# Kernel optimization log

Measured on AMD Instinct MI355X. Metric: run time of the kernel, lower is better.

The kernel has to match this reference:

```python
import jax, jax.numpy as jnp
import numpy as np

N_NODES = 100000


def _gcn_propagate(x, src, dst, n):
    """Symmetric-normalized propagation with self-loops (PyG gcn_norm, K=1).

    out[dst] += deg^-1/2[src] * deg^-1/2[dst] * x[src], including self-loops.
    """
    loop = jnp.arange(n, dtype=src.dtype)
    s = jnp.concatenate([src, loop])
    d = jnp.concatenate([dst, loop])
    deg = jax.ops.segment_sum(jnp.ones_like(d, dtype=x.dtype), d, num_segments=n)
    dinv = jnp.where(deg > 0, jax.lax.rsqrt(deg), jnp.zeros_like(deg))
    norm = dinv[s] * dinv[d]            # [E+N]
    msg = x[s] * norm[:, None]          # [E+N, F] gathered messages
    return jax.ops.segment_sum(msg, d, num_segments=n)


def setup_inputs() -> dict:
    key = jax.random.key(0)
    ks = jax.random.split(key, 6)
    n, e, f, h, c = N_NODES, 1600000, 64, 64, 16
    x = jax.random.normal(ks[0], (n, f), dtype=jnp.float32)
    edge_index = jax.random.randint(ks[1], (2, e), 0, n, dtype=jnp.int64)
    W1 = jax.random.normal(ks[2], (h, f), dtype=jnp.float32) * 0.1
    b1 = jnp.zeros((h,), dtype=jnp.float32)
    W2 = jax.random.normal(ks[3], (h, h), dtype=jnp.float32) * 0.1
    b2 = jnp.zeros((h,), dtype=jnp.float32)
    W3 = jax.random.normal(ks[4], (c, h), dtype=jnp.float32) * 0.1
    b3 = jnp.zeros((c,), dtype=jnp.float32)
    return {"x": x, "edge_index": edge_index, "W1": W1, "b1": b1,
            "W2": W2, "b2": b2, "W3": W3, "b3": b3}


def reference(x, edge_index, W1, b1, W2, b2, W3, b3):
    n = x.shape[0]
    src, dst = edge_index[0], edge_index[1]
    # SGConv 1 (K=1): propagate then linear; dropout is identity in eval mode
    h = _gcn_propagate(x, src, dst, n) @ W1.T + b1
    h = jax.nn.relu(h)
    # SGConv 2
    h = _gcn_propagate(h, src, dst, n) @ W2.T + b2
    h = jax.nn.relu(h)
    # final linear
    return h @ W3.T + b3
```

## Files before the change

### kernel.cpp

```cpp
#include <hip/hip_runtime.h>
#include <hip/hip_fp16.h>


#define F 64
#define C 16
#define SCAN_B 1024

__device__ __forceinline__ float rl(float v, int l) {
    return __uint_as_float(__builtin_amdgcn_readlane(__float_as_uint(v), l));
}

__device__ __forceinline__ float4 unpack_h4(unsigned long long raw) {
    __half2 lo = __builtin_bit_cast(__half2, (unsigned int)(raw & 0xffffffffull));
    __half2 hi = __builtin_bit_cast(__half2, (unsigned int)(raw >> 32));
    float2 f0 = __half22float2(lo);
    float2 f1 = __half22float2(hi);
    return make_float4(f0.x, f0.y, f1.x, f1.y);
}

__global__ void degrank_kernel(const int* __restrict__ dst, int* __restrict__ deg,
                               int* __restrict__ rank, int E) {
    int i = (blockIdx.x * blockDim.x + threadIdx.x) * 4;
    if (i + 4 <= E) {
        int4 d = *(const int4*)(dst + i);
        int4 r;
        r.x = atomicAdd(&deg[d.x], 1);
        r.y = atomicAdd(&deg[d.y], 1);
        r.z = atomicAdd(&deg[d.z], 1);
        r.w = atomicAdd(&deg[d.w], 1);
        *(int4*)(rank + i) = r;
    } else {
        for (int k = i; k < E; ++k) rank[k] = atomicAdd(&deg[dst[k]], 1);
    }
}

__global__ __launch_bounds__(256) void scan1_kernel(const int* __restrict__ deg,
                                                    int* __restrict__ part,
                                                    int* __restrict__ bsum, int n) {
    __shared__ int ts[256];
    int b = blockIdx.x, t = threadIdx.x;
    int base = b * SCAN_B + t * 4;
    int v[4], sum = 0;
#pragma unroll
    for (int k = 0; k < 4; ++k) { int i = base + k; v[k] = (i < n) ? deg[i] : 0; sum += v[k]; }
    ts[t] = sum;
    __syncthreads();
    for (int off = 1; off < 256; off <<= 1) {
        int add = (t >= off) ? ts[t - off] : 0;
        __syncthreads();
        ts[t] += add;
        __syncthreads();
    }
    int run = ts[t] - sum;
#pragma unroll
    for (int k = 0; k < 4; ++k) { int i = base + k; if (i < n) part[i] = run; run += v[k]; }
    if (t == 255) bsum[b] = ts[255];
}

__global__ __launch_bounds__(256) void scan2_kernel(int* __restrict__ bsum, int nb) {
    __shared__ int ts[256];
    int t = threadIdx.x;
    int v = (t < nb) ? bsum[t] : 0;
    ts[t] = v;
    __syncthreads();
    for (int off = 1; off < 256; off <<= 1) {
        int add = (t >= off) ? ts[t - off] : 0;
        __syncthreads();
        ts[t] += add;
        __syncthreads();
    }
    if (t < nb) bsum[t] = ts[t] - v;
}

__global__ void scan3_kernel(const int* __restrict__ part, const int* __restrict__ bsum,
                             const int* __restrict__ deg, int* __restrict__ rowptr,
                             float* __restrict__ dinv, int n, int E) {
    int i = blockIdx.x * blockDim.x + threadIdx.x;
    if (i < n) {
        rowptr[i] = part[i] + bsum[i / SCAN_B];
        dinv[i] = rsqrtf((float)deg[i] + 1.0f);
    }
    if (i == 0) rowptr[n] = E;
}

__global__ void fill_kernel(const int* __restrict__ src, const int* __restrict__ dst,
                            const int* __restrict__ rank, const int* __restrict__ rowptr,
                            int* __restrict__ csr_src, int E) {
    int i = (blockIdx.x * blockDim.x + threadIdx.x) * 4;
    if (i + 4 <= E) {
        int4 s = *(const int4*)(src + i);
        int4 d = *(const int4*)(dst + i);
        int4 r = *(const int4*)(rank + i);
        csr_src[rowptr[d.x] + r.x] = s.x;
        csr_src[rowptr[d.y] + r.y] = s.y;
        csr_src[rowptr[d.z] + r.z] = s.z;
        csr_src[rowptr[d.w] + r.w] = s.w;
    } else {
        for (int k = i; k < E; ++k) csr_src[rowptr[dst[k]] + rank[k]] = src[k];
    }
}

__global__ __launch_bounds__(256) void gemm1_kernel(
    const float4* __restrict__ in4, const float* __restrict__ W,
    const float* __restrict__ scale, __half* __restrict__ yout, int n) {
    int tid = threadIdx.x;
    int lane = tid & 63;
    int m = lane & 15;
    float4 w[16];
#pragma unroll
    for (int t = 0; t < 16; ++t) w[t] = *(const float4*)(W + (size_t)lane * F + 4 * t);
    int gw = blockIdx.x * 4 + (tid >> 6);
    int nw = gridDim.x * 4;
    int node = gw;
    if (node >= n) return;
    float4 v = in4[(size_t)node * 16 + m];
    while (true) {
        int nxt = node + nw;
        float4 vn;
        if (nxt < n) vn = in4[(size_t)nxt * 16 + m];
        float acc = 0.0f;
#pragma unroll
        for (int t = 0; t < 16; ++t) {
            acc = fmaf(rl(v.x, t), w[t].x, acc);
            acc = fmaf(rl(v.y, t), w[t].y, acc);
            acc = fmaf(rl(v.z, t), w[t].z, acc);
            acc = fmaf(rl(v.w, t), w[t].w, acc);
        }
        acc *= scale[node];
        yout[(size_t)node * F + lane] = __float2half(acc);
        if (nxt >= n) break;
        v = vn;
        node = nxt;
    }
}

__global__ __launch_bounds__(256) void gemm2_kernel(
    const unsigned long long* __restrict__ in8, const float* __restrict__ W,
    __half* __restrict__ yout, int n) {
    int tid = threadIdx.x;
    int lane = tid & 63;
    int m = lane & 15;
    float4 w[16];
#pragma unroll
    for (int t = 0; t < 16; ++t) w[t] = *(const float4*)(W + (size_t)lane * F + 4 * t);
    int gw = blockIdx.x * 4 + (tid >> 6);
    int nw = gridDim.x * 4;
    int node = gw;
    if (node >= n) return;
    float4 v = unpack_h4(in8[(size_t)node * 16 + m]);
    while (true) {
        int nxt = node + nw;
        float4 vn;
        if (nxt < n) vn = unpack_h4(in8[(size_t)nxt * 16 + m]);
        float acc = 0.0f;
#pragma unroll
        for (int t = 0; t < 16; ++t) {
            acc = fmaf(rl(v.x, t), w[t].x, acc);
            acc = fmaf(rl(v.y, t), w[t].y, acc);
            acc = fmaf(rl(v.z, t), w[t].z, acc);
            acc = fmaf(rl(v.w, t), w[t].w, acc);
        }
        yout[(size_t)node * F + lane] = __float2half(acc);
        if (nxt >= n) break;
        v = vn;
        node = nxt;
    }
}

#define GATHER_CORE(YTAB)                                                     \
    float4 gacc0 = {0,0,0,0}, gacc1 = {0,0,0,0};                              \
    float4 gacc2 = {0,0,0,0}, gacc3 = {0,0,0,0};                              \
    int p = beg;                                                              \
    if (p + 8 <= end) {                                                       \
        int i0 = csr_src[p],     i1 = csr_src[p + 1];                         \
        int i2 = csr_src[p + 2], i3 = csr_src[p + 3];                         \
        int i4 = csr_src[p + 4], i5 = csr_src[p + 5];                         \
        int i6 = csr_src[p + 6], i7 = csr_src[p + 7];                         \
        while (true) {                                                        \
            unsigned long long r0 = YTAB[(size_t)i0 * 16 + m];                \
            unsigned long long r1 = YTAB[(size_t)i1 * 16 + m];                \
            unsigned long long r2 = YTAB[(size_t)i2 * 16 + m];                \
            unsigned long long r3 = YTAB[(size_t)i3 * 16 + m];                \
            unsigned long long r4 = YTAB[(size_t)i4 * 16 + m];                \
            unsigned long long r5 = YTAB[(size_t)i5 * 16 + m];                \
            unsigned long long r6 = YTAB[(size_t)i6 * 16 + m];                \
            unsigned long long r7 = YTAB[(size_t)i7 * 16 + m];                \
            int np = p + 8;                                                   \
            bool more = np + 8 <= end;                                        \
            if (more) {                                                       \
                i0 = csr_src[np];     i1 = csr_src[np + 1];                   \
                i2 = csr_src[np + 2]; i3 = csr_src[np + 3];                   \
                i4 = csr_src[np + 4]; i5 = csr_src[np + 5];                   \
                i6 = csr_src[np + 6]; i7 = csr_src[np + 7];                   \
            }                                                                 \
            float4 v0 = unpack_h4(r0), v1 = unpack_h4(r1);                    \
            float4 v2 = unpack_h4(r2), v3 = unpack_h4(r3);                    \
            float4 v4 = unpack_h4(r4), v5 = unpack_h4(r5);                    \
            float4 v6 = unpack_h4(r6), v7 = unpack_h4(r7);                    \
            gacc0.x += v0.x + v4.x; gacc0.y += v0.y + v4.y;                   \
            gacc0.z += v0.z + v4.z; gacc0.w += v0.w + v4.w;                   \
            gacc1.x += v1.x + v5.x; gacc1.y += v1.y + v5.y;                   \
            gacc1.z += v1.z + v5.z; gacc1.w += v1.w + v5.w;                   \
            gacc2.x += v2.x + v6.x; gacc2.y += v2.y + v6.y;                   \
            gacc2.z += v2.z + v6.z; gacc2.w += v2.w + v6.w;                   \
            gacc3.x += v3.x + v7.x; gacc3.y += v3.y + v7.y;                   \
            gacc3.z += v3.z + v7.z; gacc3.w += v3.w + v7.w;                   \
            p = np;                                                           \
            if (!more) break;                                                 \
        }                                                                     \
    }                                                                         \
    if (p + 4 <= end) {                                                       \
        int i0 = csr_src[p], i1 = csr_src[p + 1];                             \
        int i2 = csr_src[p + 2], i3 = csr_src[p + 3];                         \
        float4 v0 = unpack_h4(YTAB[(size_t)i0 * 16 + m]);                     \
        float4 v1 = unpack_h4(YTAB[(size_t)i1 * 16 + m]);                     \
        float4 v2 = unpack_h4(YTAB[(size_t)i2 * 16 + m]);                     \
        float4 v3 = unpack_h4(YTAB[(size_t)i3 * 16 + m]);                     \
        gacc0.x += v0.x; gacc0.y += v0.y; gacc0.z += v0.z; gacc0.w += v0.w;   \
        gacc1.x += v1.x; gacc1.y += v1.y; gacc1.z += v1.z; gacc1.w += v1.w;   \
        gacc2.x += v2.x; gacc2.y += v2.y; gacc2.z += v2.z; gacc2.w += v2.w;   \
        gacc3.x += v3.x; gacc3.y += v3.y; gacc3.z += v3.z; gacc3.w += v3.w;   \
        p += 4;                                                               \
    }                                                                         \
    for (; p < end; ++p) {                                                    \
        float4 v = unpack_h4(YTAB[(size_t)csr_src[p] * 16 + m]);              \
        gacc0.x += v.x; gacc0.y += v.y; gacc0.z += v.z; gacc0.w += v.w;       \
    }                                                                         \
    float4 a;                                                                 \
    a.x = gacc0.x + gacc1.x + gacc2.x + gacc3.x;                              \
    a.y = gacc0.y + gacc1.y + gacc2.y + gacc3.y;                              \
    a.z = gacc0.z + gacc1.z + gacc2.z + gacc3.z;                              \
    a.w = gacc0.w + gacc1.w + gacc2.w + gacc3.w;

__global__ __launch_bounds__(256) void gather1_kernel(
    const unsigned long long* __restrict__ y, const int* __restrict__ rowptr,
    const int* __restrict__ csr_src, const float* __restrict__ dinv,
    const float* __restrict__ b1, __half* __restrict__ h1s, int n) {
    int tid = threadIdx.x;
    int m = tid & 15;
    float4 bias = *(const float4*)(b1 + 4 * m);
    int qid = (blockIdx.x * 256 + tid) >> 4;
    int nq = (gridDim.x * 256) >> 4;
    for (int node = qid; node < n; node += nq) {
        int beg = rowptr[node], end = rowptr[node + 1];
        GATHER_CORE(y)
        float dd = dinv[node];
        float4 self = unpack_h4(y[(size_t)node * 16 + m]);
        float4 r;
        r.x = dd * fmaxf(fmaf(dd, a.x + self.x, bias.x), 0.0f);
        r.y = dd * fmaxf(fmaf(dd, a.y + self.y, bias.y), 0.0f);
        r.z = dd * fmaxf(fmaf(dd, a.z + self.z, bias.z), 0.0f);
        r.w = dd * fmaxf(fmaf(dd, a.w + self.w, bias.w), 0.0f);
        __half2 lo = __float22half2_rn(make_float2(r.x, r.y));
        __half2 hi = __float22half2_rn(make_float2(r.z, r.w));
        float2 packed;
        packed.x = __builtin_bit_cast(float, lo);
        packed.y = __builtin_bit_cast(float, hi);
        *(float2*)(h1s + (size_t)node * F + 4 * m) = packed;
    }
}

__global__ __launch_bounds__(256) void gather2_kernel(
    const unsigned long long* __restrict__ y, const int* __restrict__ rowptr,
    const int* __restrict__ csr_src, const float* __restrict__ dinv,
    const float* __restrict__ b2, const float* __restrict__ W3,
    const float* __restrict__ b3, float* __restrict__ out, int n) {
    int tid = threadIdx.x;
    int lane = tid & 63;
    int m = lane & 15;
    int qbase = lane & 48;
    float4 bias = *(const float4*)(b2 + 4 * m);
    float b3r = b3[m];
    int qid = (blockIdx.x * 256 + tid) >> 4;
    int nq = (gridDim.x * 256) >> 4;
    for (int node = qid; node < n; node += nq) {
        int beg = rowptr[node], end = rowptr[node + 1];
        GATHER_CORE(y)
        float dd = dinv[node];
        float4 self = unpack_h4(y[(size_t)node * 16 + m]);
        float4 h;
        h.x = fmaxf(fmaf(dd, a.x + self.x, bias.x), 0.0f);
        h.y = fmaxf(fmaf(dd, a.y + self.y, bias.y), 0.0f);
        h.z = fmaxf(fmaf(dd, a.z + self.z, bias.z), 0.0f);
        h.w = fmaxf(fmaf(dd, a.w + self.w, bias.w), 0.0f);
        float acc3 = 0.0f;
#pragma unroll
        for (int t = 0; t < 16; ++t) {
            float4 wv = *(const float4*)(W3 + (size_t)m * F + 4 * t);
            float hx = __shfl(h.x, qbase + t);
            float hy = __shfl(h.y, qbase + t);
            float hz = __shfl(h.z, qbase + t);
            float hw = __shfl(h.w, qbase + t);
            acc3 = fmaf(hx, wv.x, fmaf(hy, wv.y, fmaf(hz, wv.z, fmaf(hw, wv.w, acc3))));
        }
        out[(size_t)node * C + m] = acc3 + b3r;
    }
}

extern "C" void kernel_launch(void* const* d_in, const int* in_sizes, int n_in,
                              void* d_out, int out_size, void* d_ws, size_t ws_size,
                              hipStream_t stream) {
    const float* x  = (const float*)d_in[0];
    const int* edge = (const int*)d_in[1];
    const float* W1 = (const float*)d_in[2];
    const float* b1 = (const float*)d_in[3];
    const float* W2 = (const float*)d_in[4];
    const float* b2 = (const float*)d_in[5];
    const float* W3 = (const float*)d_in[6];
    const float* b3 = (const float*)d_in[7];
    float* out = (float*)d_out;

    int n = in_sizes[0] / F;
    int E = in_sizes[1] / 2;
    const int* src = edge;
    const int* dst = edge + E;

    int nb = (n + SCAN_B - 1) / SCAN_B;

    char* ws = (char*)d_ws;
    size_t o = 0;
    auto alloc = [&](size_t bytes) { char* p = ws + o; o += (bytes + 255) & ~(size_t)255; return p; };
    int*    deg     = (int*)   alloc((size_t)n * 4);
    int*    rank    = (int*)   alloc((size_t)E * 4);
    int*    part    = (int*)   alloc((size_t)n * 4);
    int*    bsum    = (int*)   alloc(256 * 4);
    int*    rowptr  = (int*)   alloc((size_t)(n + 1) * 4);
    int*    csr_src = (int*)   alloc((size_t)E * 4);
    float*  dinv    = (float*) alloc((size_t)n * 4);
    __half* y1      = (__half*)alloc((size_t)n * F * 2);
    __half* h1s     = (__half*)alloc((size_t)n * F * 2);
    __half* y2      = y1;

    hipMemsetAsync(deg, 0, (size_t)n * 4, stream);
    degrank_kernel<<<(E / 4 + 255) / 256, 256, 0, stream>>>(dst, deg, rank, E);

    scan1_kernel<<<nb, 256, 0, stream>>>(deg, part, bsum, n);
    scan2_kernel<<<1, 256, 0, stream>>>(bsum, nb);
    scan3_kernel<<<(n + 255) / 256, 256, 0, stream>>>(part, bsum, deg, rowptr, dinv, n, E);

    gemm1_kernel<<<2048, 256, 0, stream>>>((const float4*)x, W1, dinv, y1, n);

    fill_kernel<<<(E / 4 + 255) / 256, 256, 0, stream>>>(src, dst, rank, rowptr, csr_src, E);

    gather1_kernel<<<2048, 256, 0, stream>>>(
        (const unsigned long long*)y1, rowptr, csr_src, dinv, b1, h1s, n);

    gemm2_kernel<<<2048, 256, 0, stream>>>(
        (const unsigned long long*)h1s, W2, y2, n);

    gather2_kernel<<<2048, 256, 0, stream>>>(
        (const unsigned long long*)y2, rowptr, csr_src, dinv, b2, W3, b3, out, n);
}
```

Measured before the change: 287.5 us.

## Partition CSR fill by destination range to localize scattered writes

```diff
diff --git a/kernel.cpp b/kernel.cpp
--- a/kernel.cpp
+++ b/kernel.cpp
@@ -5,6 +5,7 @@
 #define F 64
 #define C 16
 #define SCAN_B 1024
+#define NPART 8
 
 __device__ __forceinline__ float rl(float v, int l) {
     return __uint_as_float(__builtin_amdgcn_readlane(__float_as_uint(v), l));
@@ -83,20 +84,34 @@
     if (i == 0) rowptr[n] = E;
 }
 
-__global__ void fill_kernel(const int* __restrict__ src, const int* __restrict__ dst,
-                            const int* __restrict__ rank, const int* __restrict__ rowptr,
-                            int* __restrict__ csr_src, int E) {
-    int i = (blockIdx.x * blockDim.x + threadIdx.x) * 4;
-    if (i + 4 <= E) {
-        int4 s = *(const int4*)(src + i);
-        int4 d = *(const int4*)(dst + i);
-        int4 r = *(const int4*)(rank + i);
-        csr_src[rowptr[d.x] + r.x] = s.x;
-        csr_src[rowptr[d.y] + r.y] = s.y;
-        csr_src[rowptr[d.z] + r.z] = s.z;
-        csr_src[rowptr[d.w] + r.w] = s.w;
-    } else {
-        for (int k = i; k < E; ++k) csr_src[rowptr[dst[k]] + rank[k]] = src[k];
+__global__ __launch_bounds__(256) void fillp_kernel(
+    const int* __restrict__ src, const int* __restrict__ dst,
+    const int* __restrict__ rank, const int* __restrict__ rowptr,
+    int* __restrict__ csr_src, int E, int np, int n) {
+    int part = blockIdx.x & (NPART - 1);
+    int g = blockIdx.x >> 3;
+    int ng = gridDim.x >> 3;
+    int lo = part * np;
+    int hi = min(n, lo + np);
+    int stride = ng * 256 * 4;
+    for (int i = (g * 256 + threadIdx.x) * 4; i < E; i += stride) {
+        if (i + 4 <= E) {
+            int4 d = *(const int4*)(dst + i);
+            if ((d.x >= lo && d.x < hi) || (d.y >= lo && d.y < hi) ||
+                (d.z >= lo && d.z < hi) || (d.w >= lo && d.w < hi)) {
+                int4 s = *(const int4*)(src + i);
+                int4 r = *(const int4*)(rank + i);
+                if (d.x >= lo && d.x < hi) csr_src[rowptr[d.x] + r.x] = s.x;
+                if (d.y >= lo && d.y < hi) csr_src[rowptr[d.y] + r.y] = s.y;
+                if (d.z >= lo && d.z < hi) csr_src[rowptr[d.z] + r.z] = s.z;
+                if (d.w >= lo && d.w < hi) csr_src[rowptr[d.w] + r.w] = s.w;
+            }
+        } else {
+            for (int k = i; k < E; ++k) {
+                int dv = dst[k];
+                if (dv >= lo && dv < hi) csr_src[rowptr[dv] + rank[k]] = src[k];
+            }
+        }
     }
 }
 
@@ -185,13 +200,13 @@
             unsigned long long r5 = YTAB[(size_t)i5 * 16 + m];                \
             unsigned long long r6 = YTAB[(size_t)i6 * 16 + m];                \
             unsigned long long r7 = YTAB[(size_t)i7 * 16 + m];                \
-            int np = p + 8;                                                   \
-            bool more = np + 8 <= end;                                        \
+            int np_ = p + 8;                                                  \
+            bool more = np_ + 8 <= end;                                       \
             if (more) {                                                       \
-                i0 = csr_src[np];     i1 = csr_src[np + 1];                   \
-                i2 = csr_src[np + 2]; i3 = csr_src[np + 3];                   \
-                i4 = csr_src[np + 4]; i5 = csr_src[np + 5];                   \
-                i6 = csr_src[np + 6]; i7 = csr_src[np + 7];                   \
+                i0 = csr_src[np_];     i1 = csr_src[np_ + 1];                 \
+                i2 = csr_src[np_ + 2]; i3 = csr_src[np_ + 3];                 \
+                i4 = csr_src[np_ + 4]; i5 = csr_src[np_ + 5];                 \
+                i6 = csr_src[np_ + 6]; i7 = csr_src[np_ + 7];                 \
             }                                                                 \
             float4 v0 = unpack_h4(r0), v1 = unpack_h4(r1);                    \
             float4 v2 = unpack_h4(r2), v3 = unpack_h4(r3);                    \
@@ -205,7 +220,7 @@
             gacc2.z += v2.z + v6.z; gacc2.w += v2.w + v6.w;                   \
             gacc3.x += v3.x + v7.x; gacc3.y += v3.y + v7.y;                   \
             gacc3.z += v3.z + v7.z; gacc3.w += v3.w + v7.w;                   \
-            p = np;                                                           \
+            p = np_;                                                          \
             if (!more) break;                                                 \
         }                                                                     \
     }                                                                         \
@@ -316,6 +331,7 @@
     const int* dst = edge + E;
 
     int nb = (n + SCAN_B - 1) / SCAN_B;
+    int np = (n + NPART - 1) / NPART;
 
     char* ws = (char*)d_ws;
     size_t o = 0;
@@ -340,7 +356,7 @@
 
     gemm1_kernel<<<2048, 256, 0, stream>>>((const float4*)x, W1, dinv, y1, n);
 
-    fill_kernel<<<(E / 4 + 255) / 256, 256, 0, stream>>>(src, dst, rank, rowptr, csr_src, E);
+    fillp_kernel<<<2048, 256, 0, stream>>>(src, dst, rank, rowptr, csr_src, E, np, n);
 
     gather1_kernel<<<2048, 256, 0, stream>>>(
         (const unsigned long long*)y1, rowptr, csr_src, dinv, b1, h1s, n);
```

Result: no change. 292.2 us (+1.6%).
